# Performance work log

Hardware: AMD Instinct MI355X
Metric: run time of the kernel (lower is better)

## Reference

```python
import jax, jax.numpy as jnp
import numpy as np

N, F, H, T = 100000, 128, 128, 10
E = 1600000
NUM_GRAPHS = 512
BN_EPS = 1e-5


def setup_inputs() -> dict:
    key = jax.random.key(0)
    ks = jax.random.split(key, 16)
    x = jax.random.normal(ks[0], (N, F), dtype=jnp.float32)
    edge_index = jax.random.randint(ks[1], (2, E), 0, N, dtype=jnp.int64)
    batch = jnp.sort(jax.random.randint(ks[2], (N,), 0, NUM_GRAPHS, dtype=jnp.int64))
    s = lambda fin: 1.0 / np.sqrt(fin)
    return {
        "x": x, "edge_index": edge_index, "batch": batch,
        # GINConv 1 MLP: Linear(F,H) -> BN(H) -> ReLU -> Linear(H,H)
        "W1a": jax.random.uniform(ks[3], (F, H), jnp.float32, -s(F), s(F)),
        "b1a": jax.random.uniform(ks[4], (H,), jnp.float32, -s(F), s(F)),
        "g1": jnp.ones((H,), jnp.float32),
        "bt1": jnp.zeros((H,), jnp.float32),
        "W1b": jax.random.uniform(ks[5], (H, H), jnp.float32, -s(H), s(H)),
        "b1b": jax.random.uniform(ks[6], (H,), jnp.float32, -s(H), s(H)),
        # GINConv 2 MLP
        "W2a": jax.random.uniform(ks[7], (H, H), jnp.float32, -s(H), s(H)),
        "b2a": jax.random.uniform(ks[8], (H,), jnp.float32, -s(H), s(H)),
        "g2": jnp.ones((H,), jnp.float32),
        "bt2": jnp.zeros((H,), jnp.float32),
        "W2b": jax.random.uniform(ks[9], (H, H), jnp.float32, -s(H), s(H)),
        "b2b": jax.random.uniform(ks[10], (H,), jnp.float32, -s(H), s(H)),
        # final Linear(H, T)
        "Wl": jax.random.uniform(ks[11], (H, T), jnp.float32, -s(H), s(H)),
        "bl": jax.random.uniform(ks[12], (T,), jnp.float32, -s(H), s(H)),
    }


def _batchnorm(h, gamma, beta):
    # training-mode BN over the node dimension (biased variance), eps=1e-5
    mean = jnp.mean(h, axis=0)
    var = jnp.mean(jnp.square(h - mean), axis=0)
    return (h - mean) * jax.lax.rsqrt(var + BN_EPS) * gamma + beta


def _gin_conv(x, edge_index, Wa, ba, gamma, beta, Wb, bb):
    src, dst = edge_index[0], edge_index[1]
    # sum-aggregate neighbor messages: scatter-add x[src] into dst rows
    agg = jax.ops.segment_sum(x[src], dst, num_segments=x.shape[0])
    h = (x + agg) @ Wa + ba          # eps=0 in GINConv default
    h = jax.nn.relu(_batchnorm(h, gamma, beta))
    return h @ Wb + bb


def reference(x, edge_index, batch, W1a, b1a, g1, bt1, W1b, b1b,
              W2a, b2a, g2, bt2, W2b, b2b, Wl, bl):
    h = jax.nn.relu(_gin_conv(x, edge_index, W1a, b1a, g1, bt1, W1b, b1b))
    h = jax.nn.relu(_gin_conv(h, edge_index, W2a, b2a, g2, bt2, W2b, b2b))
    pooled = jax.ops.segment_sum(h, batch, num_segments=NUM_GRAPHS)  # [G, H]
    return pooled @ Wl + bl  # [G, T]
```

## Files before the change

kernel.cpp:

```cpp
#include <hip/hip_runtime.h>
#include <cstdint>
#include <cstddef>

#define NFEAT 128
#define TGRAPH 10
#define NGRAPHS 512
#define BN_EPS 1e-5f
#define BIN_CHUNK 2048
#define GSPAN 8

typedef __attribute__((ext_vector_type(8))) short bf16x8;
typedef __attribute__((ext_vector_type(4))) float f32x4;

__device__ __forceinline__ float bf2f(short s) {
    union { unsigned u; float f; } c;
    c.u = ((unsigned)(unsigned short)s) << 16;
    return c.f;
}
__device__ __forceinline__ short f2bf(float f) {
    union { float f; unsigned u; } c;
    c.f = f;
    unsigned u = c.u;
    return (short)((u + 0x7fffu + ((u >> 16) & 1u)) >> 16);
}
__device__ __forceinline__ void acc2(float& a, float& b, unsigned v) {
    union { unsigned u; float f; } lo, hi;
    lo.u = v << 16;
    hi.u = v & 0xffff0000u;
    a += lo.f;
    b += hi.f;
}


__global__ __launch_bounds__(256) void k_bucket_hist(const int* __restrict__ dst,
                                                     int* __restrict__ bhist, int E) {
    __shared__ int h[256];
    int t = threadIdx.x;
    h[t] = 0;
    __syncthreads();
    for (int e = blockIdx.x * blockDim.x + t; e < E; e += gridDim.x * blockDim.x)
        atomicAdd(&h[dst[e] >> 9], 1);
    __syncthreads();
    if (h[t]) atomicAdd(&bhist[t], h[t]);
}

__global__ void k_bucket_scan(const int* __restrict__ bhist, int* __restrict__ bbase,
                              int* __restrict__ cur256, int E) {
    __shared__ int s[256];
    int t = threadIdx.x;
    int v = bhist[t];
    s[t] = v;
    __syncthreads();
    for (int off = 1; off < 256; off <<= 1) {
        int x = 0;
        if (t >= off) x = s[t - off];
        __syncthreads();
        if (t >= off) s[t] += x;
        __syncthreads();
    }
    int excl = s[t] - v;
    bbase[t] = excl;
    cur256[t] = excl;
    if (t == 255) bbase[256] = E;
}

__global__ __launch_bounds__(256) void k_bin_scatter(const int* __restrict__ src,
                                                     const int* __restrict__ dst,
                                                     int* __restrict__ cur256,
                                                     int2* __restrict__ binned, int E) {
    __shared__ int hist[256];
    __shared__ int base[256];
    int t = threadIdx.x;
    int e0 = blockIdx.x * BIN_CHUNK;
    int e1 = min(e0 + BIN_CHUNK, E);
    hist[t] = 0;
    __syncthreads();
    for (int e = e0 + t; e < e1; e += 256) {
        int b = dst[e] >> 9;
        atomicAdd(&hist[b], 1);
    }
    __syncthreads();
    int c = hist[t];
    if (c > 0) base[t] = atomicAdd(&cur256[t], c);
    __syncthreads();
    hist[t] = 0;
    __syncthreads();
    for (int e = e0 + t; e < e1; e += 256) {
        int d = dst[e];
        int b = d >> 9;
        int loc = atomicAdd(&hist[b], 1);
        binned[base[b] + loc] = make_int2(src[e], d);
    }
}

__global__ __launch_bounds__(512) void k_bucket_csr(const int2* __restrict__ binned,
                                                    const int* __restrict__ bbase,
                                                    int* __restrict__ rowptr,
                                                    int* __restrict__ adj,
                                                    int N, int E, int nb) {
    __shared__ int deg[512];
    __shared__ int cur[512];
    int b = blockIdx.x;
    int t = threadIdx.x;
    int e0 = bbase[b], e1 = bbase[b + 1];
    deg[t] = 0;
    __syncthreads();
    for (int e = e0 + t; e < e1; e += 512)
        atomicAdd(&deg[binned[e].y & 511], 1);
    __syncthreads();
    int v = deg[t];
    for (int off = 1; off < 512; off <<= 1) {
        int x = 0;
        if (t >= off) x = deg[t - off];
        __syncthreads();
        if (t >= off) deg[t] += x;
        __syncthreads();
    }
    int excl = deg[t] - v;
    cur[t] = excl;
    int node = b * 512 + t;
    if (node < N) rowptr[node] = e0 + excl;
    if (b == nb - 1 && t == 0) rowptr[N] = E;
    __syncthreads();
    for (int e = e0 + t; e < e1; e += 512) {
        int2 p = binned[e];
        int loc = atomicAdd(&cur[p.y & 511], 1);
        adj[e0 + loc] = p.x;
    }
}

__global__ void k_prep(const float* __restrict__ x, short* __restrict__ xbf,
                       const float* __restrict__ W0, const float* __restrict__ W1,
                       const float* __restrict__ W2, const float* __restrict__ W3,
                       short* __restrict__ Wf, int n4) {
    int i = blockIdx.x * blockDim.x + threadIdx.x;
    if (i < n4) {
        float4 v = ((const float4*)x)[i];
        ushort4 o;
        o.x = (unsigned short)f2bf(v.x);
        o.y = (unsigned short)f2bf(v.y);
        o.z = (unsigned short)f2bf(v.z);
        o.w = (unsigned short)f2bf(v.w);
        ((ushort4*)xbf)[i] = o;
    } else {
        int idx = i - n4;
        if (idx < 4 * 16384) {
            int w = idx >> 14, r = idx & 16383;
            int j = r & 7, lane = (r >> 3) & 63, ct = (r >> 9) & 7, kc = r >> 12;
            int k = kc * 32 + (lane >> 4) * 8 + j;
            int n = ct * 16 + (lane & 15);
            const float* W = (w == 0) ? W0 : (w == 1) ? W1 : (w == 2) ? W2 : W3;
            Wf[idx] = f2bf(W[k * NFEAT + n]);
        }
    }
}

__global__ __launch_bounds__(256) void k_aggregate_v4(const short* __restrict__ X,
                                                      const int* __restrict__ rowptr,
                                                      const int* __restrict__ adj,
                                                      short* __restrict__ XA, int N) {
    int tid = threadIdx.x;
    int lane = tid & 63;
    int g = lane >> 4;
    int p = lane & 15;
    int wid = (blockIdx.x * blockDim.x + tid) >> 6;
    if (wid >= N) return;
    const uint4* Xv = (const uint4*)X;
    float acc[8];
#pragma unroll
    for (int j = 0; j < 8; j++) acc[j] = 0.f;
    int r0 = rowptr[wid], r1 = rowptr[wid + 1];
    for (int e = r0; e < r1; e += 16) {
        int ea = e + g, eb = e + 4 + g, ec = e + 8 + g, ed = e + 12 + g;
        uint4 v0 = {0u, 0u, 0u, 0u}, v1 = {0u, 0u, 0u, 0u};
        uint4 v2 = {0u, 0u, 0u, 0u}, v3 = {0u, 0u, 0u, 0u};
        if (ea < r1) v0 = Xv[(size_t)adj[ea] * 16 + p];
        if (eb < r1) v1 = Xv[(size_t)adj[eb] * 16 + p];
        if (ec < r1) v2 = Xv[(size_t)adj[ec] * 16 + p];
        if (ed < r1) v3 = Xv[(size_t)adj[ed] * 16 + p];
        acc2(acc[0], acc[1], v0.x); acc2(acc[2], acc[3], v0.y);
        acc2(acc[4], acc[5], v0.z); acc2(acc[6], acc[7], v0.w);
        acc2(acc[0], acc[1], v1.x); acc2(acc[2], acc[3], v1.y);
        acc2(acc[4], acc[5], v1.z); acc2(acc[6], acc[7], v1.w);
        acc2(acc[0], acc[1], v2.x); acc2(acc[2], acc[3], v2.y);
        acc2(acc[4], acc[5], v2.z); acc2(acc[6], acc[7], v2.w);
        acc2(acc[0], acc[1], v3.x); acc2(acc[2], acc[3], v3.y);
        acc2(acc[4], acc[5], v3.z); acc2(acc[6], acc[7], v3.w);
    }
#pragma unroll
    for (int j = 0; j < 8; j++) {
        acc[j] += __shfl_xor(acc[j], 16);
        acc[j] += __shfl_xor(acc[j], 32);
    }
    if (g == 0) {
        uint4 sv = Xv[(size_t)wid * 16 + p];
        acc2(acc[0], acc[1], sv.x); acc2(acc[2], acc[3], sv.y);
        acc2(acc[4], acc[5], sv.z); acc2(acc[6], acc[7], sv.w);
        uint4 o;
        o.x = (unsigned)(unsigned short)f2bf(acc[0]) | ((unsigned)(unsigned short)f2bf(acc[1]) << 16);
        o.y = (unsigned)(unsigned short)f2bf(acc[2]) | ((unsigned)(unsigned short)f2bf(acc[3]) << 16);
        o.z = (unsigned)(unsigned short)f2bf(acc[4]) | ((unsigned)(unsigned short)f2bf(acc[5]) << 16);
        o.w = (unsigned)(unsigned short)f2bf(acc[6]) | ((unsigned)(unsigned short)f2bf(acc[7]) << 16);
        size_t dst = ((size_t)(wid >> 4) * 4 + (p >> 2)) * 512 +
                     (size_t)(((p & 3) * 16 + (wid & 15)) * 8);
        *(uint4*)(XA + dst) = o;
    }
}

template <bool BN_RELU_IN, bool RELU_OUT, bool STATS, bool FRAG_OUT, bool POOL>
__global__ __launch_bounds__(256) void k_gemm_mfma(const short* __restrict__ A,
                                                   const short* __restrict__ Wf,
                                                   const float* __restrict__ bias,
                                                   float* __restrict__ stats,
                                                   const float* __restrict__ gamma,
                                                   const float* __restrict__ beta,
                                                   const int* __restrict__ batch,
                                                   float* __restrict__ pooled,
                                                   short* __restrict__ C, int N) {
    __shared__ float s_aux[256];
    __shared__ short c_tile[4][512];
    __shared__ float s_pool[GSPAN][NFEAT];
    int tid = threadIdx.x;
    int wave = tid >> 6, lane = tid & 63;
    int quad = lane >> 4, l16 = lane & 15;
    int row_base = blockIdx.x * 128 + wave * 32;

    int gbase = 0;
    if constexpr (POOL) {
        int first = blockIdx.x * 128;
        gbase = (first < N) ? batch[first] : 0;
        for (int i = tid; i < GSPAN * NFEAT; i += 256) s_pool[i >> 7][i & 127] = 0.f;
    }
    if constexpr (STATS) s_aux[tid] = 0.f;
    if constexpr (BN_RELU_IN) {
        if (tid < NFEAT) {
            float mean = stats[tid] / (float)N;
            float var = stats[NFEAT + tid] / (float)N - mean * mean;
            float inv = rsqrtf(var + BN_EPS);
            float sc = gamma[tid] * inv;
            s_aux[tid] = sc;
            s_aux[NFEAT + tid] = beta[tid] - mean * sc;
        }
    }
    if constexpr (STATS || BN_RELU_IN || POOL) __syncthreads();

    f32x4 acc[2][8];
#pragma unroll
    for (int i = 0; i < 2; i++)
#pragma unroll
        for (int j = 0; j < 8; j++) acc[i][j] = (f32x4){0.f, 0.f, 0.f, 0.f};

    const short* af = A + ((size_t)(blockIdx.x * 8 + wave * 2) * 4) * 512;

#pragma unroll
    for (int kc = 0; kc < 4; ++kc) {
        bf16x8 a0 = *(const bf16x8*)(af + (size_t)kc * 512 + lane * 8);
        bf16x8 a1 = *(const bf16x8*)(af + (size_t)(4 + kc) * 512 + lane * 8);
        if constexpr (BN_RELU_IN) {
            int koff = kc * 32 + quad * 8;
#pragma unroll
            for (int j = 0; j < 8; j++) {
                float sc = s_aux[koff + j];
                float sh = s_aux[NFEAT + koff + j];
                a0[j] = f2bf(fmaxf(bf2f(a0[j]) * sc + sh, 0.f));
                a1[j] = f2bf(fmaxf(bf2f(a1[j]) * sc + sh, 0.f));
            }
        }
        const short* wp = Wf + ((size_t)(kc * 8) * 64 + lane) * 8;
#pragma unroll
        for (int ct = 0; ct < 8; ++ct) {
            bf16x8 b = *(const bf16x8*)(wp + (size_t)ct * 64 * 8);
            acc[0][ct] = __builtin_amdgcn_mfma_f32_16x16x32_bf16(a0, b, acc[0][ct], 0, 0, 0);
            acc[1][ct] = __builtin_amdgcn_mfma_f32_16x16x32_bf16(a1, b, acc[1][ct], 0, 0, 0);
        }
    }

    int dg[8];
    if constexpr (POOL) {
#pragma unroll
        for (int rt = 0; rt < 2; ++rt)
#pragma unroll
            for (int reg = 0; reg < 4; ++reg) {
                int row = row_base + rt * 16 + quad * 4 + reg;
                dg[rt * 4 + reg] = (row < N) ? (batch[row] - gbase) : -1;
            }
    }

    short* tile = &c_tile[wave][0];
    int row2 = lane >> 1, half = lane & 1;
#pragma unroll
    for (int ct = 0; ct < 8; ++ct) {
        int col = ct * 16 + l16;
        float bv = bias[col];
        float ls = 0.f, ls2 = 0.f;
        int cg = -1;
        float ps = 0.f;
#pragma unroll
        for (int rt = 0; rt < 2; ++rt) {
#pragma unroll
            for (int reg = 0; reg < 4; ++reg) {
                int lrow = rt * 16 + quad * 4 + reg;
                float v = acc[rt][ct][reg] + bv;
                if constexpr (RELU_OUT) v = fmaxf(v, 0.f);
                if constexpr (STATS) {
                    if (row_base + lrow < N) { ls += v; ls2 += v * v; }
                }
                if constexpr (POOL) {
                    int d = dg[rt * 4 + reg];
                    if (d != cg) {
                        if (cg >= 0) atomicAdd(&s_pool[cg & (GSPAN - 1)][col], ps);
                        cg = d; ps = 0.f;
                    }
                    if (d >= 0) ps += v;
                } else {
                    tile[lrow * 16 + l16] = f2bf(v);
                }
            }
        }
        if constexpr (POOL) {
            if (cg >= 0) atomicAdd(&s_pool[cg & (GSPAN - 1)][col], ps);
        }
        if constexpr (STATS) {
            ls += __shfl_xor(ls, 16);
            ls += __shfl_xor(ls, 32);
            ls2 += __shfl_xor(ls2, 16);
            ls2 += __shfl_xor(ls2, 32);
            if (quad == 0) {
                atomicAdd(&s_aux[col], ls);
                atomicAdd(&s_aux[NFEAT + col], ls2);
            }
        }
        if constexpr (!POOL) {
            uint4 val = *(const uint4*)(tile + row2 * 16 + half * 8);
            int grow = row_base + row2;
            if (grow < N) {
                int col0 = ct * 16 + half * 8;
                if constexpr (FRAG_OUT) {
                    size_t addr = ((size_t)(grow >> 4) * 4 + (col0 >> 5)) * 512 +
                                  (size_t)((((col0 >> 3) & 3) * 16 + (grow & 15)) * 8);
                    *(uint4*)(C + addr) = val;
                } else {
                    *(uint4*)(C + (size_t)grow * NFEAT + col0) = val;
                }
            }
        }
    }

    if constexpr (STATS) {
        __syncthreads();
        if (tid < NFEAT) {
            atomicAdd(&stats[tid], s_aux[tid]);
            atomicAdd(&stats[NFEAT + tid], s_aux[NFEAT + tid]);
        }
    }
    if constexpr (POOL) {
        __syncthreads();
        for (int i = tid; i < GSPAN * NFEAT; i += 256) {
            float v = s_pool[i >> 7][i & 127];
            if (v != 0.f) {
                int gg = gbase + (i >> 7);
                if (gg < NGRAPHS) atomicAdd(&pooled[gg * NFEAT + (i & 127)], v);
            }
        }
    }
}

__global__ void k_final(const float* __restrict__ pooled, const float* __restrict__ Wl,
                        const float* __restrict__ bl, float* __restrict__ out) {
    int idx = blockIdx.x * blockDim.x + threadIdx.x;
    if (idx >= NGRAPHS * TGRAPH) return;
    int g = idx / TGRAPH, t = idx % TGRAPH;
    const float* p = pooled + (size_t)g * NFEAT;
    float acc = bl[t];
#pragma unroll 16
    for (int k = 0; k < NFEAT; ++k) acc += p[k] * Wl[k * TGRAPH + t];
    out[idx] = acc;
}

extern "C" void kernel_launch(void* const* d_in, const int* in_sizes, int n_in,
                              void* d_out, int out_size, void* d_ws, size_t ws_size,
                              hipStream_t stream) {
    const float* x = (const float*)d_in[0];
    const int* ei = (const int*)d_in[1];
    const int* batch = (const int*)d_in[2];
    const float* W1a = (const float*)d_in[3];
    const float* b1a = (const float*)d_in[4];
    const float* g1 = (const float*)d_in[5];
    const float* bt1 = (const float*)d_in[6];
    const float* W1b = (const float*)d_in[7];
    const float* b1b = (const float*)d_in[8];
    const float* W2a = (const float*)d_in[9];
    const float* b2a = (const float*)d_in[10];
    const float* g2 = (const float*)d_in[11];
    const float* bt2 = (const float*)d_in[12];
    const float* W2b = (const float*)d_in[13];
    const float* b2b = (const float*)d_in[14];
    const float* Wl = (const float*)d_in[15];
    const float* bl = (const float*)d_in[16];
    float* out = (float*)d_out;

    int N = in_sizes[2];
    int E = in_sizes[1] / 2;
    int nb = (N + 511) >> 9;
    const int* src = ei;
    const int* dst = ei + E;

    int gemmBlocks = (N + 127) / 128;
    int padRows = gemmBlocks * 128;

    char* ws = (char*)d_ws;
    size_t off = 0;
    auto alloc = [&](size_t bytes) -> void* {
        void* p = ws + off;
        off = (off + bytes + 255) & ~(size_t)255;
        return p;
    };
    short* xbf = (short*)alloc((size_t)N * NFEAT * 2);
    short* ag = (short*)alloc((size_t)padRows * NFEAT * 2);
    short* ybf = (short*)alloc((size_t)padRows * NFEAT * 2);
    short* hbf = (short*)alloc((size_t)N * NFEAT * 2);
    short* Wf = (short*)alloc((size_t)4 * 16384 * 2);
    int* adj = (int*)alloc((size_t)E * 4);
    int2* binned = (int2*)alloc((size_t)E * 8);
    int* rowptr = (int*)alloc((size_t)(N + 1) * 4);
    int* bbase = (int*)alloc(257 * 4);
    int* cur256 = (int*)alloc(256 * 4);
    int* bhist = (int*)alloc(256 * 4);
    float* stats1 = (float*)alloc(256 * 4);
    float* stats2 = (float*)alloc(256 * 4);
    float* pooled = (float*)alloc((size_t)NGRAPHS * NFEAT * 4);
    size_t zbytes = (char*)(pooled + (size_t)NGRAPHS * NFEAT) - (char*)bhist;

    hipMemsetAsync(bhist, 0, zbytes, stream);

    k_bucket_hist<<<784, 256, 0, stream>>>(dst, bhist, E);
    k_bucket_scan<<<1, 256, 0, stream>>>(bhist, bbase, cur256, E);
    k_bin_scatter<<<(E + BIN_CHUNK - 1) / BIN_CHUNK, 256, 0, stream>>>(src, dst, cur256, binned, E);
    k_bucket_csr<<<nb, 512, 0, stream>>>(binned, bbase, rowptr, adj, N, E, nb);

    int n4 = N * NFEAT / 4;
    int prepTot = n4 + 4 * 16384;
    k_prep<<<(prepTot + 255) / 256, 256, 0, stream>>>(x, xbf, W1a, W1b, W2a, W2b, Wf, n4);

    int aggBlocks = (N + 3) / 4;

    k_aggregate_v4<<<aggBlocks, 256, 0, stream>>>(xbf, rowptr, adj, ag, N);
    k_gemm_mfma<false, false, true, true, false><<<gemmBlocks, 256, 0, stream>>>(
        ag, Wf + 0 * 16384, b1a, stats1, nullptr, nullptr, nullptr, nullptr, ybf, N);
    k_gemm_mfma<true, true, false, false, false><<<gemmBlocks, 256, 0, stream>>>(
        ybf, Wf + 1 * 16384, b1b, stats1, g1, bt1, nullptr, nullptr, hbf, N);

    k_aggregate_v4<<<aggBlocks, 256, 0, stream>>>(hbf, rowptr, adj, ag, N);
    k_gemm_mfma<false, false, true, true, false><<<gemmBlocks, 256, 0, stream>>>(
        ag, Wf + 2 * 16384, b2a, stats2, nullptr, nullptr, nullptr, nullptr, ybf, N);
    k_gemm_mfma<true, true, false, false, true><<<gemmBlocks, 256, 0, stream>>>(
        ybf, Wf + 3 * 16384, b2b, stats2, g2, bt2, batch, pooled, nullptr, N);

    k_final<<<(NGRAPHS * TGRAPH + 255) / 256, 256, 0, stream>>>(pooled, Wl, bl, out);
}
```

Before: 457.8 us.

## Fuse histogram into prep kernel, pack aggregation accumulators, pad GEMM output tile

```diff
diff --git a/kernel.cpp b/kernel.cpp
--- a/kernel.cpp
+++ b/kernel.cpp
@@ -8,9 +8,11 @@
 #define BN_EPS 1e-5f
 #define BIN_CHUNK 2048
 #define GSPAN 8
+#define TSTR 24
 
 typedef __attribute__((ext_vector_type(8))) short bf16x8;
 typedef __attribute__((ext_vector_type(4))) float f32x4;
+typedef __attribute__((ext_vector_type(2))) float f32x2;
 
 __device__ __forceinline__ float bf2f(short s) {
     union { unsigned u; float f; } c;
@@ -23,26 +25,16 @@
     unsigned u = c.u;
     return (short)((u + 0x7fffu + ((u >> 16) & 1u)) >> 16);
 }
-__device__ __forceinline__ void acc2(float& a, float& b, unsigned v) {
+__device__ __forceinline__ void accp(f32x2& a, unsigned v) {
     union { unsigned u; float f; } lo, hi;
     lo.u = v << 16;
     hi.u = v & 0xffff0000u;
-    a += lo.f;
-    b += hi.f;
-}
-
-
-__global__ __launch_bounds__(256) void k_bucket_hist(const int* __restrict__ dst,
-                                                     int* __restrict__ bhist, int E) {
-    __shared__ int h[256];
-    int t = threadIdx.x;
-    h[t] = 0;
-    __syncthreads();
-    for (int e = blockIdx.x * blockDim.x + t; e < E; e += gridDim.x * blockDim.x)
-        atomicAdd(&h[dst[e] >> 9], 1);
-    __syncthreads();
-    if (h[t]) atomicAdd(&bhist[t], h[t]);
-}
+    f32x2 t;
+    t[0] = lo.f;
+    t[1] = hi.f;
+    a += t;
+}
+
 
 __global__ void k_bucket_scan(const int* __restrict__ bhist, int* __restrict__ bbase,
                               int* __restrict__ cur256, int E) {
@@ -129,11 +121,27 @@
     }
 }
 
-__global__ void k_prep(const float* __restrict__ x, short* __restrict__ xbf,
-                       const float* __restrict__ W0, const float* __restrict__ W1,
-                       const float* __restrict__ W2, const float* __restrict__ W3,
-                       short* __restrict__ Wf, int n4) {
-    int i = blockIdx.x * blockDim.x + threadIdx.x;
+__global__ __launch_bounds__(256) void k_prep_hist(const int* __restrict__ dst,
+                                                   int* __restrict__ bhist, int E, int hb,
+                                                   const float* __restrict__ x,
+                                                   short* __restrict__ xbf,
+                                                   const float* __restrict__ W0,
+                                                   const float* __restrict__ W1,
+                                                   const float* __restrict__ W2,
+                                                   const float* __restrict__ W3,
+                                                   short* __restrict__ Wf, int n4) {
+    int t = threadIdx.x;
+    if (blockIdx.x < hb) {
+        __shared__ int h[256];
+        h[t] = 0;
+        __syncthreads();
+        for (int e = blockIdx.x * 256 + t; e < E; e += hb * 256)
+            atomicAdd(&h[dst[e] >> 9], 1);
+        __syncthreads();
+        if (h[t]) atomicAdd(&bhist[t], h[t]);
+        return;
+    }
+    int i = (blockIdx.x - hb) * 256 + t;
     if (i < n4) {
         float4 v = ((const float4*)x)[i];
         ushort4 o;
@@ -166,9 +174,9 @@
     int wid = (blockIdx.x * blockDim.x + tid) >> 6;
     if (wid >= N) return;
     const uint4* Xv = (const uint4*)X;
-    float acc[8];
-#pragma unroll
-    for (int j = 0; j < 8; j++) acc[j] = 0.f;
+    f32x2 ac[4];
+#pragma unroll
+    for (int j = 0; j < 4; j++) ac[j] = (f32x2){0.f, 0.f};
     int r0 = rowptr[wid], r1 = rowptr[wid + 1];
     for (int e = r0; e < r1; e += 16) {
         int ea = e + g, eb = e + 4 + g, ec = e + 8 + g, ed = e + 12 + g;
@@ -178,29 +186,26 @@
         if (eb < r1) v1 = Xv[(size_t)adj[eb] * 16 + p];
         if (ec < r1) v2 = Xv[(size_t)adj[ec] * 16 + p];
         if (ed < r1) v3 = Xv[(size_t)adj[ed] * 16 + p];
-        acc2(acc[0], acc[1], v0.x); acc2(acc[2], acc[3], v0.y);
-        acc2(acc[4], acc[5], v0.z); acc2(acc[6], acc[7], v0.w);
-        acc2(acc[0], acc[1], v1.x); acc2(acc[2], acc[3], v1.y);
-        acc2(acc[4], acc[5], v1.z); acc2(acc[6], acc[7], v1.w);
-        acc2(acc[0], acc[1], v2.x); acc2(acc[2], acc[3], v2.y);
-        acc2(acc[4], acc[5], v2.z); acc2(acc[6], acc[7], v2.w);
-        acc2(acc[0], acc[1], v3.x); acc2(acc[2], acc[3], v3.y);
-        acc2(acc[4], acc[5], v3.z); acc2(acc[6], acc[7], v3.w);
-    }
-#pragma unroll
-    for (int j = 0; j < 8; j++) {
-        acc[j] += __shfl_xor(acc[j], 16);
-        acc[j] += __shfl_xor(acc[j], 32);
+        accp(ac[0], v0.x); accp(ac[1], v0.y); accp(ac[2], v0.z); accp(ac[3], v0.w);
+        accp(ac[0], v1.x); accp(ac[1], v1.y); accp(ac[2], v1.z); accp(ac[3], v1.w);
+        accp(ac[0], v2.x); accp(ac[1], v2.y); accp(ac[2], v2.z); accp(ac[3], v2.w);
+        accp(ac[0], v3.x); accp(ac[1], v3.y); accp(ac[2], v3.z); accp(ac[3], v3.w);
+    }
+#pragma unroll
+    for (int j = 0; j < 4; j++) {
+        ac[j][0] += __shfl_xor(ac[j][0], 16);
+        ac[j][1] += __shfl_xor(ac[j][1], 16);
+        ac[j][0] += __shfl_xor(ac[j][0], 32);
+        ac[j][1] += __shfl_xor(ac[j][1], 32);
     }
     if (g == 0) {
         uint4 sv = Xv[(size_t)wid * 16 + p];
-        acc2(acc[0], acc[1], sv.x); acc2(acc[2], acc[3], sv.y);
-        acc2(acc[4], acc[5], sv.z); acc2(acc[6], acc[7], sv.w);
+        accp(ac[0], sv.x); accp(ac[1], sv.y); accp(ac[2], sv.z); accp(ac[3], sv.w);
         uint4 o;
-        o.x = (unsigned)(unsigned short)f2bf(acc[0]) | ((unsigned)(unsigned short)f2bf(acc[1]) << 16);
-        o.y = (unsigned)(unsigned short)f2bf(acc[2]) | ((unsigned)(unsigned short)f2bf(acc[3]) << 16);
-        o.z = (unsigned)(unsigned short)f2bf(acc[4]) | ((unsigned)(unsigned short)f2bf(acc[5]) << 16);
-        o.w = (unsigned)(unsigned short)f2bf(acc[6]) | ((unsigned)(unsigned short)f2bf(acc[7]) << 16);
+        o.x = (unsigned)(unsigned short)f2bf(ac[0][0]) | ((unsigned)(unsigned short)f2bf(ac[0][1]) << 16);
+        o.y = (unsigned)(unsigned short)f2bf(ac[1][0]) | ((unsigned)(unsigned short)f2bf(ac[1][1]) << 16);
+        o.z = (unsigned)(unsigned short)f2bf(ac[2][0]) | ((unsigned)(unsigned short)f2bf(ac[2][1]) << 16);
+        o.w = (unsigned)(unsigned short)f2bf(ac[3][0]) | ((unsigned)(unsigned short)f2bf(ac[3][1]) << 16);
         size_t dst = ((size_t)(wid >> 4) * 4 + (p >> 2)) * 512 +
                      (size_t)(((p & 3) * 16 + (wid & 15)) * 8);
         *(uint4*)(XA + dst) = o;
@@ -218,7 +223,7 @@
                                                    float* __restrict__ pooled,
                                                    short* __restrict__ C, int N) {
     __shared__ float s_aux[256];
-    __shared__ short c_tile[4][512];
+    __shared__ short c_tile[4][32 * TSTR];
     __shared__ float s_pool[GSPAN][NFEAT];
     int tid = threadIdx.x;
     int wave = tid >> 6, lane = tid & 63;
@@ -313,7 +318,7 @@
                     }
                     if (d >= 0) ps += v;
                 } else {
-                    tile[lrow * 16 + l16] = f2bf(v);
+                    tile[lrow * TSTR + l16] = f2bf(v);
                 }
             }
         }
@@ -331,7 +336,7 @@
             }
         }
         if constexpr (!POOL) {
-            uint4 val = *(const uint4*)(tile + row2 * 16 + half * 8);
+            uint4 val = *(const uint4*)(tile + row2 * TSTR + half * 8);
             int grow = row_base + row2;
             if (grow < N) {
                 int col0 = ct * 16 + half * 8;
@@ -433,14 +438,14 @@
 
     hipMemsetAsync(bhist, 0, zbytes, stream);
 
-    k_bucket_hist<<<784, 256, 0, stream>>>(dst, bhist, E);
+    int n4 = N * NFEAT / 4;
+    int prepTot = n4 + 4 * 16384;
+    int hb = 784;
+    k_prep_hist<<<hb + (prepTot + 255) / 256, 256, 0, stream>>>(
+        dst, bhist, E, hb, x, xbf, W1a, W1b, W2a, W2b, Wf, n4);
     k_bucket_scan<<<1, 256, 0, stream>>>(bhist, bbase, cur256, E);
     k_bin_scatter<<<(E + BIN_CHUNK - 1) / BIN_CHUNK, 256, 0, stream>>>(src, dst, cur256, binned, E);
     k_bucket_csr<<<nb, 512, 0, stream>>>(binned, bbase, rowptr, adj, N, E, nb);
-
-    int n4 = N * NFEAT / 4;
-    int prepTot = n4 + 4 * 16384;
-    k_prep<<<(prepTot + 255) / 256, 256, 0, stream>>>(x, xbf, W1a, W1b, W2a, W2b, Wf, n4);
 
     int aggBlocks = (N + 3) / 4;
 
```

After: 438.4 us. 4.2% less time.
